# Optimization experiments

Measured on AMD Instinct MI355X. Metric: run time of the kernel, lower is better.

Reference implementation:

```python
import jax, jax.numpy as jnp
import numpy as np

N = 50000      # nodes
E = 800000     # edges (avg degree 16)
G = 256        # graphs in batch
F = 128        # num_node_features
H = 128        # graph_hidden_channels
NHID = 256
NOUT = 128


def setup_inputs() -> dict:
    key = jax.random.key(0)
    ks = jax.random.split(key, 16)
    s = 0.05
    x = jax.random.normal(ks[0], (N, F), dtype=jnp.float32)
    edge_index = jax.random.randint(ks[1], (2, E), 0, N, dtype=jnp.int64)
    batch = jnp.sort(jax.random.randint(ks[2], (N,), 0, G, dtype=jnp.int64))
    return {
        "x": x,
        "edge_index": edge_index,
        "batch": batch,
        # GCNConv: lin weight + bias
        "W0": jax.random.normal(ks[3], (F, H), dtype=jnp.float32) * s,
        "b0": jnp.zeros((H,), dtype=jnp.float32),
        # GIN layer 1 and 2 (eps=0, nn = Linear)
        "Wg1": jax.random.normal(ks[4], (H, H), dtype=jnp.float32) * s,
        "bg1": jnp.zeros((H,), dtype=jnp.float32),
        "Wg2": jax.random.normal(ks[5], (H, H), dtype=jnp.float32) * s,
        "bg2": jnp.zeros((H,), dtype=jnp.float32),
        # mol_hidden1 / mol_hidden2
        "Wh1": jax.random.normal(ks[6], (H, NHID), dtype=jnp.float32) * s,
        "bh1": jnp.zeros((NHID,), dtype=jnp.float32),
        "Wh2": jax.random.normal(ks[7], (NHID, NOUT), dtype=jnp.float32) * s,
        "bh2": jnp.zeros((NOUT,), dtype=jnp.float32),
    }


def reference(x, edge_index, batch, W0, b0, Wg1, bg1, Wg2, bg2, Wh1, bh1, Wh2, bh2):
    src, dst = edge_index[0], edge_index[1]
    loop = jnp.arange(N, dtype=src.dtype)
    src_sl = jnp.concatenate([src, loop])   # with self-loops (GCN)
    dst_sl = jnp.concatenate([dst, loop])

    # --- GCNConv: sym-normalized aggregation with self-loops ---
    deg = jax.ops.segment_sum(jnp.ones_like(dst_sl, dtype=x.dtype), dst_sl, num_segments=N)
    dinv = jax.lax.rsqrt(jnp.maximum(deg, 1.0))  # deg >= 1 because of self-loops
    norm = dinv[src_sl] * dinv[dst_sl]           # [E+N]
    h = x @ W0                                   # [N, H]
    h = jax.ops.segment_sum(h[src_sl] * norm[:, None], dst_sl, num_segments=N) + b0
    h = jax.nn.relu(h)

    # --- GIN layers: Linear((1+eps)*x + sum_neighbors), eps=0, no self-loops ---
    for Wg, bg in ((Wg1, bg1), (Wg2, bg2)):
        agg = jax.ops.segment_sum(h[src], dst, num_segments=N)  # sum aggregation
        h = jax.nn.relu((h + agg) @ Wg + bg)

    # --- global mean pool per graph, then MLP head ---
    s = jax.ops.segment_sum(h, batch, num_segments=G)                       # [G, H]
    cnt = jax.ops.segment_sum(jnp.ones((N,), dtype=h.dtype), batch, num_segments=G)
    m = s / jnp.maximum(cnt, 1.0)[:, None]
    g = jax.nn.relu(m @ Wh1 + bh1)   # mol_hidden1 + relu
    out = g @ Wh2 + bh2              # mol_hidden2
    return out
```

## Files before the change

### kernel.cpp

```cpp
#include <hip/hip_runtime.h>


__global__ void count_kernel(const int* __restrict__ dst, int* __restrict__ cnt, int E) {
    int e = blockIdx.x * blockDim.x + threadIdx.x;
    if (e < E) atomicAdd(&cnt[dst[e]], 1);
}

__global__ void scan1(const int* __restrict__ cnt, int* __restrict__ offs,
                      int* __restrict__ partials, int N) {
    __shared__ int s[256];
    int t = threadIdx.x;
    int i = blockIdx.x * 256 + t;
    int v = (i < N) ? cnt[i] : 0;
    s[t] = v;
    __syncthreads();
    #pragma unroll
    for (int d = 1; d < 256; d <<= 1) {
        int tv = (t >= d) ? s[t - d] : 0;
        __syncthreads();
        s[t] += tv;
        __syncthreads();
    }
    if (i < N) offs[i] = s[t] - v;
    if (t == 255) partials[blockIdx.x] = s[255];
}

__global__ void scan2(int* partials, int nb) {
    __shared__ int s[256];
    int t = threadIdx.x;
    int v = (t < nb) ? partials[t] : 0;
    s[t] = v;
    __syncthreads();
    #pragma unroll
    for (int d = 1; d < 256; d <<= 1) {
        int tv = (t >= d) ? s[t - d] : 0;
        __syncthreads();
        s[t] += tv;
        __syncthreads();
    }
    if (t < nb) partials[t] = s[t] - v;
}

__global__ void scan3(const int* __restrict__ cnt, int* __restrict__ offs,
                      int* __restrict__ offwork, float* __restrict__ dinv,
                      const int* __restrict__ partials, int N, int E) {
    int i = blockIdx.x * 256 + threadIdx.x;
    if (i < N) {
        int o = offs[i] + partials[blockIdx.x];
        offs[i] = o;
        offwork[i] = o;
        dinv[i] = rsqrtf((float)cnt[i] + 1.0f);
    }
    if (i == 0) offs[N] = E;
}

__global__ void scatter_kernel(const int* __restrict__ src, const int* __restrict__ dst,
                               int* __restrict__ offwork, int* __restrict__ csr, int E) {
    int e = blockIdx.x * blockDim.x + threadIdx.x;
    if (e < E) {
        int pos = atomicAdd(&offwork[dst[e]], 1);
        csr[pos] = src[e];
    }
}


__global__ __launch_bounds__(256, 2) void gemm128(const float* __restrict__ X,
                                                  const float* __restrict__ W,
                                                  const float* __restrict__ bias,
                                                  float* __restrict__ Y,
                                                  int M, int relu) {
    __shared__ float As[32][68];
    __shared__ float Bs[32][132];

    int tid = threadIdx.x;
    int tx = tid & 15;
    int ty = tid >> 4;
    int row0 = blockIdx.x * 64;

    float acc[4][8];
    #pragma unroll
    for (int r = 0; r < 4; r++)
        #pragma unroll
        for (int c = 0; c < 8; c++) acc[r][c] = 0.0f;

    int lr = tid >> 2;
    int kc = (tid & 3) * 8;
    int wr = tid >> 3;
    int wc = (tid & 7) * 16;

    for (int k0 = 0; k0 < 128; k0 += 32) {
        float4 xa, xb;
        int grow = row0 + lr;
        if (grow < M) {
            xa = *(const float4*)&X[grow * 128 + k0 + kc];
            xb = *(const float4*)&X[grow * 128 + k0 + kc + 4];
        } else {
            xa = make_float4(0.f, 0.f, 0.f, 0.f);
            xb = make_float4(0.f, 0.f, 0.f, 0.f);
        }
        float4 w0 = *(const float4*)&W[(k0 + wr) * 128 + wc + 0];
        float4 w1 = *(const float4*)&W[(k0 + wr) * 128 + wc + 4];
        float4 w2 = *(const float4*)&W[(k0 + wr) * 128 + wc + 8];
        float4 w3 = *(const float4*)&W[(k0 + wr) * 128 + wc + 12];

        __syncthreads();
        As[kc + 0][lr] = xa.x; As[kc + 1][lr] = xa.y;
        As[kc + 2][lr] = xa.z; As[kc + 3][lr] = xa.w;
        As[kc + 4][lr] = xb.x; As[kc + 5][lr] = xb.y;
        As[kc + 6][lr] = xb.z; As[kc + 7][lr] = xb.w;
        *(float4*)&Bs[wr][wc + 0]  = w0;
        *(float4*)&Bs[wr][wc + 4]  = w1;
        *(float4*)&Bs[wr][wc + 8]  = w2;
        *(float4*)&Bs[wr][wc + 12] = w3;
        __syncthreads();

        #pragma unroll
        for (int k = 0; k < 32; k++) {
            float4 a   = *(const float4*)&As[k][ty * 4];
            float4 bb0 = *(const float4*)&Bs[k][tx * 4];
            float4 bb1 = *(const float4*)&Bs[k][64 + tx * 4];
            float av[4] = {a.x, a.y, a.z, a.w};
            float bv[8] = {bb0.x, bb0.y, bb0.z, bb0.w, bb1.x, bb1.y, bb1.z, bb1.w};
            #pragma unroll
            for (int r = 0; r < 4; r++)
                #pragma unroll
                for (int c = 0; c < 8; c++)
                    acc[r][c] = fmaf(av[r], bv[c], acc[r][c]);
        }
    }

    #pragma unroll
    for (int r = 0; r < 4; r++) {
        int grow = row0 + ty * 4 + r;
        if (grow < M) {
            float o[8];
            #pragma unroll
            for (int c = 0; c < 8; c++) o[c] = acc[r][c];
            if (bias) {
                #pragma unroll
                for (int c = 0; c < 4; c++) {
                    o[c]     += bias[tx * 4 + c];
                    o[c + 4] += bias[64 + tx * 4 + c];
                }
            }
            if (relu) {
                #pragma unroll
                for (int c = 0; c < 8; c++) o[c] = fmaxf(o[c], 0.0f);
            }
            float4 o0 = make_float4(o[0], o[1], o[2], o[3]);
            float4 o1 = make_float4(o[4], o[5], o[6], o[7]);
            *(float4*)&Y[grow * 128 + tx * 4]      = o0;
            *(float4*)&Y[grow * 128 + 64 + tx * 4] = o1;
        }
    }
}


__global__ void gcn_agg(const float* __restrict__ A, float* __restrict__ B,
                        const int* __restrict__ offs, const int* __restrict__ csr,
                        const float* __restrict__ dinv, const float* __restrict__ b0) {
    int v = blockIdx.x;
    int f = threadIdx.x;
    float dv = dinv[v];
    float acc = A[v * 128 + f] * dv;
    int i0 = offs[v], i1 = offs[v + 1];
    for (int i = i0; i < i1; i++) {
        int s = csr[i];
        acc += A[s * 128 + f] * dinv[s];
    }
    float r = acc * dv + b0[f];
    B[v * 128 + f] = fmaxf(r, 0.0f);
}

__global__ void gin_agg(const float* __restrict__ H, float* __restrict__ U,
                        const int* __restrict__ offs, const int* __restrict__ csr) {
    int v = blockIdx.x;
    int f = threadIdx.x;
    float acc = H[v * 128 + f];
    int i0 = offs[v], i1 = offs[v + 1];
    for (int i = i0; i < i1; i++) {
        acc += H[csr[i] * 128 + f];
    }
    U[v * 128 + f] = acc;
}


__global__ void graph_bounds(const int* __restrict__ batch, int* __restrict__ gstart,
                             int N, int G) {
    int g = blockIdx.x * blockDim.x + threadIdx.x;
    if (g > G) return;
    int lo = 0, hi = N;
    while (lo < hi) {
        int mid = (lo + hi) >> 1;
        if (batch[mid] < g) lo = mid + 1; else hi = mid;
    }
    gstart[g] = lo;
}

__global__ void pool_kernel(const float* __restrict__ H, const int* __restrict__ gstart,
                            float* __restrict__ Mout) {
    int g = blockIdx.x;
    int f = threadIdx.x;
    int s = gstart[g], e = gstart[g + 1];
    float acc = 0.0f;
    for (int i = s; i < e; i++) acc += H[i * 128 + f];
    int n = e - s;
    Mout[g * 128 + f] = acc / (float)(n > 0 ? n : 1);
}

__global__ void head1(const float* __restrict__ Mx, const float* __restrict__ W,
                      const float* __restrict__ b, float* __restrict__ Y) {
    __shared__ float m[128];
    int g = blockIdx.x;
    int j = threadIdx.x;
    if (j < 128) m[j] = Mx[g * 128 + j];
    __syncthreads();
    float acc = b[j];
    for (int k = 0; k < 128; k++) acc = fmaf(m[k], W[k * 256 + j], acc);
    Y[g * 256 + j] = fmaxf(acc, 0.0f);
}

__global__ void head2(const float* __restrict__ Gx, const float* __restrict__ W,
                      const float* __restrict__ b, float* __restrict__ out) {
    __shared__ float m[256];
    int g = blockIdx.x;
    int j = threadIdx.x;
    m[j] = Gx[g * 256 + j];
    m[j + 128] = Gx[g * 256 + 128 + j];
    __syncthreads();
    float acc = b[j];
    for (int k = 0; k < 256; k++) acc = fmaf(m[k], W[k * 128 + j], acc);
    out[g * 128 + j] = acc;
}


extern "C" void kernel_launch(void* const* d_in, const int* in_sizes, int n_in,
                              void* d_out, int out_size, void* d_ws, size_t ws_size,
                              hipStream_t stream) {
    const float* x     = (const float*)d_in[0];
    const int*   ei    = (const int*)d_in[1];
    const int*   batch = (const int*)d_in[2];
    const float* W0  = (const float*)d_in[3];
    const float* b0  = (const float*)d_in[4];
    const float* Wg1 = (const float*)d_in[5];
    const float* bg1 = (const float*)d_in[6];
    const float* Wg2 = (const float*)d_in[7];
    const float* bg2 = (const float*)d_in[8];
    const float* Wh1 = (const float*)d_in[9];
    const float* bh1 = (const float*)d_in[10];
    const float* Wh2 = (const float*)d_in[11];
    const float* bh2 = (const float*)d_in[12];

    int N = in_sizes[2];
    int E = in_sizes[1] / 2;
    int G = out_size / 128;
    const int* srcp = ei;
    const int* dstp = ei + E;

    char* w = (char*)d_ws;
    auto take = [&](size_t bytes) -> void* {
        void* p = (void*)w;
        w += (bytes + 255) & ~(size_t)255;
        return p;
    };
    float* A        = (float*)take((size_t)N * 128 * 4);
    float* Bf       = (float*)take((size_t)N * 128 * 4);
    int*   csr      = (int*)take((size_t)E * 4);
    int*   offs     = (int*)take((size_t)(N + 1) * 4);
    int*   offw     = (int*)take((size_t)N * 4);
    int*   cnt      = (int*)take((size_t)N * 4);
    float* dinv     = (float*)take((size_t)N * 4);
    int*   partials = (int*)take(1024);
    int*   gstart   = (int*)take((size_t)(G + 1) * 4);
    float* Mg       = (float*)take((size_t)G * 128 * 4);
    float* Gh       = (float*)take((size_t)G * 256 * 4);

    int nb = (N + 255) / 256;

    hipMemsetAsync(cnt, 0, (size_t)N * 4, stream);
    count_kernel<<<(E + 255) / 256, 256, 0, stream>>>(dstp, cnt, E);
    scan1<<<nb, 256, 0, stream>>>(cnt, offs, partials, N);
    scan2<<<1, 256, 0, stream>>>(partials, nb);
    scan3<<<nb, 256, 0, stream>>>(cnt, offs, offw, dinv, partials, N, E);
    scatter_kernel<<<(E + 255) / 256, 256, 0, stream>>>(srcp, dstp, offw, csr, E);

    gemm128<<<(N + 63) / 64, 256, 0, stream>>>(x, W0, nullptr, A, N, 0);
    gcn_agg<<<N, 128, 0, stream>>>(A, Bf, offs, csr, dinv, b0);

    gin_agg<<<N, 128, 0, stream>>>(Bf, A, offs, csr);
    gemm128<<<(N + 63) / 64, 256, 0, stream>>>(A, Wg1, bg1, Bf, N, 1);

    gin_agg<<<N, 128, 0, stream>>>(Bf, A, offs, csr);
    gemm128<<<(N + 63) / 64, 256, 0, stream>>>(A, Wg2, bg2, Bf, N, 1);

    graph_bounds<<<(G + 1 + 255) / 256, 256, 0, stream>>>(batch, gstart, N, G);
    pool_kernel<<<G, 128, 0, stream>>>(Bf, gstart, Mg);
    head1<<<G, 256, 0, stream>>>(Mg, Wh1, bh1, Gh);
    head2<<<G, 128, 0, stream>>>(Gh, Wh2, bh2, (float*)d_out);
}
```

Before: 610.8 us.

## Prescale GCN rows in GEMM, vectorize and unroll aggregation, parallelize mean pooling

Folds the source-side dinv scaling into the first GEMM epilogue, so GCN aggregation no longer gathers dinv per edge. GCN and GIN aggregation now use float2 loads with 64 lanes per node, two nodes per block, and an 8-way unrolled neighbor loop to raise memory-level parallelism. Mean pooling becomes a row-chunked partial sum with atomics, with the divide moved into head1, instead of one block per graph scanning rows serially. The head matvec loops are unrolled. In exchange, pooling order becomes nondeterministic through float atomics and an extra memset is needed.

```diff
diff --git a/kernel.cpp b/kernel.cpp
--- a/kernel.cpp
+++ b/kernel.cpp
@@ -67,6 +67,7 @@
 __global__ __launch_bounds__(256, 2) void gemm128(const float* __restrict__ X,
                                                   const float* __restrict__ W,
                                                   const float* __restrict__ bias,
+                                                  const float* __restrict__ rowscale,
                                                   float* __restrict__ Y,
                                                   int M, int relu) {
     __shared__ float As[32][68];
@@ -133,6 +134,7 @@
     for (int r = 0; r < 4; r++) {
         int grow = row0 + ty * 4 + r;
         if (grow < M) {
+            float scale = rowscale ? rowscale[grow] : 1.0f;
             float o[8];
             #pragma unroll
             for (int c = 0; c < 8; c++) o[c] = acc[r][c];
@@ -143,6 +145,8 @@
                     o[c + 4] += bias[64 + tx * 4 + c];
                 }
             }
+            #pragma unroll
+            for (int c = 0; c < 8; c++) o[c] *= scale;
             if (relu) {
                 #pragma unroll
                 for (int c = 0; c < 8; c++) o[c] = fmaxf(o[c], 0.0f);
@@ -158,30 +162,78 @@
 
 __global__ void gcn_agg(const float* __restrict__ A, float* __restrict__ B,
                         const int* __restrict__ offs, const int* __restrict__ csr,
-                        const float* __restrict__ dinv, const float* __restrict__ b0) {
-    int v = blockIdx.x;
-    int f = threadIdx.x;
+                        const float* __restrict__ dinv, const float* __restrict__ b0,
+                        int N) {
+    int v = blockIdx.x * 2 + (threadIdx.x >> 6);
+    if (v >= N) return;
+    int lane = threadIdx.x & 63;
+    const float2* Ap = (const float2*)A;
+    float2 acc = Ap[v * 64 + lane];
+    int i0 = offs[v], i1 = offs[v + 1];
+    int i = i0;
+    for (; i + 8 <= i1; i += 8) {
+        int s0 = csr[i + 0], s1 = csr[i + 1], s2 = csr[i + 2], s3 = csr[i + 3];
+        int s4 = csr[i + 4], s5 = csr[i + 5], s6 = csr[i + 6], s7 = csr[i + 7];
+        float2 a0 = Ap[s0 * 64 + lane], a1 = Ap[s1 * 64 + lane];
+        float2 a2 = Ap[s2 * 64 + lane], a3 = Ap[s3 * 64 + lane];
+        float2 a4 = Ap[s4 * 64 + lane], a5 = Ap[s5 * 64 + lane];
+        float2 a6 = Ap[s6 * 64 + lane], a7 = Ap[s7 * 64 + lane];
+        acc.x += a0.x + a1.x + a2.x + a3.x + a4.x + a5.x + a6.x + a7.x;
+        acc.y += a0.y + a1.y + a2.y + a3.y + a4.y + a5.y + a6.y + a7.y;
+    }
+    for (; i + 4 <= i1; i += 4) {
+        int s0 = csr[i + 0], s1 = csr[i + 1], s2 = csr[i + 2], s3 = csr[i + 3];
+        float2 a0 = Ap[s0 * 64 + lane], a1 = Ap[s1 * 64 + lane];
+        float2 a2 = Ap[s2 * 64 + lane], a3 = Ap[s3 * 64 + lane];
+        acc.x += a0.x + a1.x + a2.x + a3.x;
+        acc.y += a0.y + a1.y + a2.y + a3.y;
+    }
+    for (; i < i1; i++) {
+        float2 a = Ap[csr[i] * 64 + lane];
+        acc.x += a.x;
+        acc.y += a.y;
+    }
     float dv = dinv[v];
-    float acc = A[v * 128 + f] * dv;
+    float2 bb = ((const float2*)b0)[lane];
+    float2 r;
+    r.x = fmaxf(acc.x * dv + bb.x, 0.0f);
+    r.y = fmaxf(acc.y * dv + bb.y, 0.0f);
+    ((float2*)B)[v * 64 + lane] = r;
+}
+
+__global__ void gin_agg(const float* __restrict__ H, float* __restrict__ U,
+                        const int* __restrict__ offs, const int* __restrict__ csr,
+                        int N) {
+    int v = blockIdx.x * 2 + (threadIdx.x >> 6);
+    if (v >= N) return;
+    int lane = threadIdx.x & 63;
+    const float2* Hp = (const float2*)H;
+    float2 acc = Hp[v * 64 + lane];
     int i0 = offs[v], i1 = offs[v + 1];
-    for (int i = i0; i < i1; i++) {
-        int s = csr[i];
-        acc += A[s * 128 + f] * dinv[s];
-    }
-    float r = acc * dv + b0[f];
-    B[v * 128 + f] = fmaxf(r, 0.0f);
-}
-
-__global__ void gin_agg(const float* __restrict__ H, float* __restrict__ U,
-                        const int* __restrict__ offs, const int* __restrict__ csr) {
-    int v = blockIdx.x;
-    int f = threadIdx.x;
-    float acc = H[v * 128 + f];
-    int i0 = offs[v], i1 = offs[v + 1];
-    for (int i = i0; i < i1; i++) {
-        acc += H[csr[i] * 128 + f];
-    }
-    U[v * 128 + f] = acc;
+    int i = i0;
+    for (; i + 8 <= i1; i += 8) {
+        int s0 = csr[i + 0], s1 = csr[i + 1], s2 = csr[i + 2], s3 = csr[i + 3];
+        int s4 = csr[i + 4], s5 = csr[i + 5], s6 = csr[i + 6], s7 = csr[i + 7];
+        float2 a0 = Hp[s0 * 64 + lane], a1 = Hp[s1 * 64 + lane];
+        float2 a2 = Hp[s2 * 64 + lane], a3 = Hp[s3 * 64 + lane];
+        float2 a4 = Hp[s4 * 64 + lane], a5 = Hp[s5 * 64 + lane];
+        float2 a6 = Hp[s6 * 64 + lane], a7 = Hp[s7 * 64 + lane];
+        acc.x += a0.x + a1.x + a2.x + a3.x + a4.x + a5.x + a6.x + a7.x;
+        acc.y += a0.y + a1.y + a2.y + a3.y + a4.y + a5.y + a6.y + a7.y;
+    }
+    for (; i + 4 <= i1; i += 4) {
+        int s0 = csr[i + 0], s1 = csr[i + 1], s2 = csr[i + 2], s3 = csr[i + 3];
+        float2 a0 = Hp[s0 * 64 + lane], a1 = Hp[s1 * 64 + lane];
+        float2 a2 = Hp[s2 * 64 + lane], a3 = Hp[s3 * 64 + lane];
+        acc.x += a0.x + a1.x + a2.x + a3.x;
+        acc.y += a0.y + a1.y + a2.y + a3.y;
+    }
+    for (; i < i1; i++) {
+        float2 a = Hp[csr[i] * 64 + lane];
+        acc.x += a.x;
+        acc.y += a.y;
+    }
+    ((float2*)U)[v * 64 + lane] = acc;
 }
 
 
@@ -197,25 +249,38 @@
     gstart[g] = lo;
 }
 
-__global__ void pool_kernel(const float* __restrict__ H, const int* __restrict__ gstart,
-                            float* __restrict__ Mout) {
-    int g = blockIdx.x;
-    int f = threadIdx.x;
-    int s = gstart[g], e = gstart[g + 1];
+__global__ void pool_partial(const float* __restrict__ H, const int* __restrict__ batch,
+                             float* __restrict__ S, int N) {
+    int r0 = blockIdx.x * 128;
+    int r1 = min(r0 + 128, N);
+    if (r0 >= N) return;
+    int t = threadIdx.x;
     float acc = 0.0f;
-    for (int i = s; i < e; i++) acc += H[i * 128 + f];
-    int n = e - s;
-    Mout[g * 128 + f] = acc / (float)(n > 0 ? n : 1);
-}
-
-__global__ void head1(const float* __restrict__ Mx, const float* __restrict__ W,
-                      const float* __restrict__ b, float* __restrict__ Y) {
+    int curg = batch[r0];
+    for (int r = r0; r < r1; r++) {
+        int g = batch[r];
+        if (g != curg) {
+            atomicAdd(&S[curg * 128 + t], acc);
+            acc = 0.0f;
+            curg = g;
+        }
+        acc += H[r * 128 + t];
+    }
+    atomicAdd(&S[curg * 128 + t], acc);
+}
+
+__global__ void head1(const float* __restrict__ S, const int* __restrict__ gstart,
+                      const float* __restrict__ W, const float* __restrict__ b,
+                      float* __restrict__ Y) {
     __shared__ float m[128];
     int g = blockIdx.x;
     int j = threadIdx.x;
-    if (j < 128) m[j] = Mx[g * 128 + j];
+    int n = gstart[g + 1] - gstart[g];
+    float inv = 1.0f / (float)(n > 0 ? n : 1);
+    if (j < 128) m[j] = S[g * 128 + j] * inv;
     __syncthreads();
     float acc = b[j];
+    #pragma unroll 8
     for (int k = 0; k < 128; k++) acc = fmaf(m[k], W[k * 256 + j], acc);
     Y[g * 256 + j] = fmaxf(acc, 0.0f);
 }
@@ -229,6 +294,7 @@
     m[j + 128] = Gx[g * 256 + 128 + j];
     __syncthreads();
     float acc = b[j];
+    #pragma unroll 8
     for (int k = 0; k < 256; k++) acc = fmaf(m[k], W[k * 128 + j], acc);
     out[g * 128 + j] = acc;
 }
@@ -272,29 +338,30 @@
     float* dinv     = (float*)take((size_t)N * 4);
     int*   partials = (int*)take(1024);
     int*   gstart   = (int*)take((size_t)(G + 1) * 4);
-    float* Mg       = (float*)take((size_t)G * 128 * 4);
+    float* S        = (float*)take((size_t)G * 128 * 4);
     float* Gh       = (float*)take((size_t)G * 256 * 4);
 
     int nb = (N + 255) / 256;
 
     hipMemsetAsync(cnt, 0, (size_t)N * 4, stream);
+    hipMemsetAsync(S, 0, (size_t)G * 128 * 4, stream);
     count_kernel<<<(E + 255) / 256, 256, 0, stream>>>(dstp, cnt, E);
     scan1<<<nb, 256, 0, stream>>>(cnt, offs, partials, N);
     scan2<<<1, 256, 0, stream>>>(partials, nb);
     scan3<<<nb, 256, 0, stream>>>(cnt, offs, offw, dinv, partials, N, E);
     scatter_kernel<<<(E + 255) / 256, 256, 0, stream>>>(srcp, dstp, offw, csr, E);
 
-    gemm128<<<(N + 63) / 64, 256, 0, stream>>>(x, W0, nullptr, A, N, 0);
-    gcn_agg<<<N, 128, 0, stream>>>(A, Bf, offs, csr, dinv, b0);
-
-    gin_agg<<<N, 128, 0, stream>>>(Bf, A, offs, csr);
-    gemm128<<<(N + 63) / 64, 256, 0, stream>>>(A, Wg1, bg1, Bf, N, 1);
-
-    gin_agg<<<N, 128, 0, stream>>>(Bf, A, offs, csr);
-    gemm128<<<(N + 63) / 64, 256, 0, stream>>>(A, Wg2, bg2, Bf, N, 1);
+    gemm128<<<(N + 63) / 64, 256, 0, stream>>>(x, W0, nullptr, dinv, A, N, 0);
+    gcn_agg<<<(N + 1) / 2, 128, 0, stream>>>(A, Bf, offs, csr, dinv, b0, N);
+
+    gin_agg<<<(N + 1) / 2, 128, 0, stream>>>(Bf, A, offs, csr, N);
+    gemm128<<<(N + 63) / 64, 256, 0, stream>>>(A, Wg1, bg1, nullptr, Bf, N, 1);
+
+    gin_agg<<<(N + 1) / 2, 128, 0, stream>>>(Bf, A, offs, csr, N);
+    gemm128<<<(N + 63) / 64, 256, 0, stream>>>(A, Wg2, bg2, nullptr, Bf, N, 1);
 
     graph_bounds<<<(G + 1 + 255) / 256, 256, 0, stream>>>(batch, gstart, N, G);
-    pool_kernel<<<G, 128, 0, stream>>>(Bf, gstart, Mg);
-    head1<<<G, 256, 0, stream>>>(Mg, Wh1, bh1, Gh);
+    pool_partial<<<(N + 127) / 128, 128, 0, stream>>>(Bf, batch, S, N);
+    head1<<<G, 256, 0, stream>>>(S, gstart, Wh1, bh1, Gh);
     head2<<<G, 128, 0, stream>>>(Gh, Wh2, bh2, (float*)d_out);
 }
```

Measured after the change: 497.7 us. 18.5% less time.
